# Optimization experiments

Hardware: AMD Instinct MI355X
Metric: run time of the kernel (lower is better)

The kernel has to match this reference:

```python
import jax, jax.numpy as jnp
import numpy as np

EMBED = 768
HEADS = 12
HEAD_DIM = EMBED // HEADS
RANK = 16
EPS = 1e-6
SCALE = 1.0 / np.sqrt(HEAD_DIM)


def setup_inputs() -> dict:
    key = jax.random.key(0)
    ks = jax.random.split(key, 12)
    B, S = 4, 1024
    hidden_states = jax.random.normal(ks[0], (B, S, EMBED), dtype=jnp.float32)
    attention_mask = jnp.zeros((B, 1, 1, S), dtype=jnp.float32)
    w = lambda k: jax.random.normal(k, (EMBED, EMBED), dtype=jnp.float32) * 0.02
    b = lambda k: jax.random.normal(k, (EMBED,), dtype=jnp.float32) * 0.02
    A = jax.random.normal(ks[9], (HEADS, HEAD_DIM, RANK), dtype=jnp.float32) * 0.05
    return {
        "hidden_states": hidden_states,
        "attention_mask": attention_mask,
        "Wq": w(ks[1]), "bq": b(ks[2]),
        "Wk": w(ks[3]), "bk": b(ks[4]),
        "Wv": w(ks[5]), "bv": b(ks[6]),
        "Wo": w(ks[7]), "bo": b(ks[8]),
        "A": A,
    }


def reference(hidden_states, attention_mask, Wq, bq, Wk, bk, Wv, bv, Wo, bo, A):
    B, S, E = hidden_states.shape
    H, D = HEADS, HEAD_DIM

    def proj(W, bias):
        y = hidden_states @ W.T + bias          # (B,S,E), torch Linear: x W^T + b
        return y.reshape(B, S, H, D).transpose(0, 2, 1, 3)  # (B,H,S,D)

    q = proj(Wq, bq)
    k = proj(Wk, bk)
    v = proj(Wv, bv)

    # Low-rank SPD Mahalanobis: G_h = A_h A_h^T + eps*I
    # d^2(x,y) = ||A^T(x-y)||^2 + eps*||x-y||^2 (block-diagonal per batch)
    qA = jnp.einsum("bhsd,hdr->bhsr", q, A)    # (B,H,S,R)
    kA = jnp.einsum("bhsd,hdr->bhsr", k, A)
    qq = jnp.sum(qA * qA, -1) + EPS * jnp.sum(q * q, -1)  # (B,H,S)
    kk = jnp.sum(kA * kA, -1) + EPS * jnp.sum(k * k, -1)
    cross = jnp.einsum("bhsr,bhtr->bhst", qA, kA) + EPS * jnp.einsum("bhsd,bhtd->bhst", q, k)
    d2 = qq[..., :, None] + kk[..., None, :] - 2.0 * cross  # (B,H,S,S)

    scores = -d2 * SCALE + attention_mask      # mask broadcasts (B,1,1,S)
    weights = jax.nn.softmax(scores, axis=-1)  # dropout p is identity in eval
    ctx = jnp.einsum("bhst,bhtd->bhsd", weights, v)
    ctx = ctx.transpose(0, 2, 1, 3).reshape(B, S, E)
    return ctx @ Wo.T + bo
```

## Files before the change

kernel.cpp:

```cpp
#include <hip/hip_runtime.h>

typedef __attribute__((ext_vector_type(8))) short s16x8;
typedef __attribute__((ext_vector_type(4))) float f32x4;
typedef __attribute__((ext_vector_type(4))) unsigned int u32x4;
typedef __attribute__((ext_vector_type(2))) unsigned int u32x2;
typedef unsigned short u16;
typedef unsigned int u32;
typedef unsigned long long u64;

__device__ __forceinline__ u16 f2bf(float f) {
  u32 u = __float_as_uint(f);
  u32 r = u + 0x7fffu + ((u >> 16) & 1u);
  return (u16)(r >> 16);
}
__device__ __forceinline__ float bf2f(u16 h) {
  return __uint_as_float(((u32)h) << 16);
}

typedef __attribute__((address_space(3))) char lds_char_t;
typedef __attribute__((address_space(1))) const char glb_char_t;
__device__ __forceinline__ void gl2lds16(const void* g, void* l) {
  __builtin_amdgcn_global_load_lds((glb_char_t*)g, (lds_char_t*)l, 16, 0, 0);
}

#define HS_N 3145728
#define W_N  589824
#define LOG2E 1.44269504f

__global__ __launch_bounds__(256) void convert_kernel(
    const float* __restrict__ hs, const float* __restrict__ wq, const float* __restrict__ wk,
    const float* __restrict__ wv, const float* __restrict__ wo,
    const float* __restrict__ bq, const float* __restrict__ bk, const float* __restrict__ bv,
    u16* __restrict__ hsb, u16* __restrict__ wqkvb, u16* __restrict__ wob,
    float* __restrict__ biasqkv)
{
  int t = blockIdx.x * 256 + threadIdx.x;
  long i = (long)t * 8;
  const float* src;
  u16* dst;
  if (i < HS_N)              { src = hs + i;                  dst = hsb + i; }
  else if (i < HS_N + W_N)   { src = wq + (i - HS_N);         dst = wqkvb + (i - HS_N); }
  else if (i < HS_N + 2*W_N) { src = wk + (i - HS_N - W_N);   dst = wqkvb + (i - HS_N); }
  else if (i < HS_N + 3*W_N) { src = wv + (i - HS_N - 2*W_N); dst = wqkvb + (i - HS_N); }
  else                       { src = wo + (i - HS_N - 3*W_N); dst = wob + (i - HS_N - 3*W_N); }
  float4 a = ((const float4*)src)[0];
  float4 b = ((const float4*)src)[1];
  uint4 o;
  o.x = (u32)f2bf(a.x) | ((u32)f2bf(a.y) << 16);
  o.y = (u32)f2bf(a.z) | ((u32)f2bf(a.w) << 16);
  o.z = (u32)f2bf(b.x) | ((u32)f2bf(b.y) << 16);
  o.w = (u32)f2bf(b.z) | ((u32)f2bf(b.w) << 16);
  *(uint4*)dst = o;
  if (t < 2304) biasqkv[t] = (t < 768) ? bq[t] : ((t < 1536) ? bk[t - 768] : bv[t - 1536]);
}

template<int MODE>
__global__ __launch_bounds__(256, 2) void gemm_bt(
    const u16* __restrict__ A, const u16* __restrict__ Bt, const float* __restrict__ bias,
    float* __restrict__ outF, u16* __restrict__ Qb, u16* __restrict__ Kb, u16* __restrict__ Vtb)
{
  constexpr int NT = (MODE == 0) ? 18 : 6;
  constexpr int CPX = NT * 64 / 8;

  __shared__ __align__(16) char sm[73728];
  char* const smA = sm;
  char* const smB = sm + 24576;

  const int tid = threadIdx.x;
  const int lane = tid & 63;
  const int w = tid >> 6;
  const int l15 = lane & 15, g = lane >> 4;
  const int wid = (blockIdx.x & 7) * CPX + (blockIdx.x >> 3);
  const int bx = wid % NT, by = wid / NT;
  const int mBase = by * 64;
  const int nBase = bx * 128;
  const int wr = w >> 1, wc = w & 1;
  const int mW = wr * 32, nW = wc * 64;

  f32x4 zero = {0.f, 0.f, 0.f, 0.f};
  f32x4 acc[2][4];
  #pragma unroll
  for (int i = 0; i < 2; i++)
    #pragma unroll
    for (int j = 0; j < 4; j++) acc[i][j] = zero;

  const u16* Arow = A + (long)mBase * 768;
  const u16* Brow = Bt + (long)nBase * 768;

  auto stage = [&](int c, int kb) {
    const int k0 = c * 64;
    #pragma unroll
    for (int i = 0; i < 2; i++) {
      int o = (i * 256 + tid) * 16;
      int r = o >> 7;
      int sl = ((o >> 4) & 7) ^ (r & 7);
      gl2lds16(Arow + (long)r * 768 + k0 + sl * 8,
               smA + kb * 8192 + i * 4096 + w * 1024);
    }
    #pragma unroll
    for (int i = 0; i < 4; i++) {
      int o = (i * 256 + tid) * 16;
      int r = o >> 7;
      int sl = ((o >> 4) & 7) ^ (r & 7);
      gl2lds16(Brow + (long)r * 768 + k0 + sl * 8,
               smB + kb * 16384 + i * 4096 + w * 1024);
    }
  };

  auto compute = [&](int kb) {
    const char* bufA = smA + kb * 8192;
    const char* bufB = smB + kb * 16384;
    #pragma unroll
    for (int kh = 0; kh < 2; kh++) {
      s16x8 af[2], bf[4];
      #pragma unroll
      for (int mi = 0; mi < 2; mi++) {
        int R = mW + mi * 16 + l15;
        af[mi] = *(const s16x8*)(bufA + R * 128 + (((kh * 4 + g) ^ (l15 & 7)) << 4));
      }
      #pragma unroll
      for (int ni = 0; ni < 4; ni++) {
        int R = nW + ni * 16 + l15;
        bf[ni] = *(const s16x8*)(bufB + R * 128 + (((kh * 4 + g) ^ (l15 & 7)) << 4));
      }
      #pragma unroll
      for (int mi = 0; mi < 2; mi++)
        #pragma unroll
        for (int ni = 0; ni < 4; ni++)
          acc[mi][ni] = __builtin_amdgcn_mfma_f32_16x16x32_bf16(af[mi], bf[ni], acc[mi][ni], 0, 0, 0);
    }
  };

  auto body = [&](int c, int kb, int kbn) {
    if (c < 11) { stage(c + 1, kbn); asm volatile("s_waitcnt vmcnt(6)" ::: "memory"); }
    else        { asm volatile("s_waitcnt vmcnt(0)" ::: "memory"); }
    asm volatile("s_barrier" ::: "memory");
    compute(kb);
  };

  stage(0, 0);
  #pragma unroll 1
  for (int cc = 0; cc < 4; cc++) {
    body(cc * 3,     0, 1);
    body(cc * 3 + 1, 1, 2);
    body(cc * 3 + 2, 2, 0);
  }
  __syncthreads();

  const int b_ = mBase >> 10;
  const int s0b = mBase & 1023;

  if constexpr (MODE == 1) {
    #pragma unroll
    for (int mi = 0; mi < 2; mi++)
      #pragma unroll
      for (int ni = 0; ni < 4; ni++) {
        int n = nBase + nW + ni * 16 + l15;
        int m0 = mBase + mW + mi * 16 + g * 4;
        float bb = bias[n];
        outF[(long)m0 * 768 + n]       = acc[mi][ni][0] + bb;
        outF[(long)(m0 + 1) * 768 + n] = acc[mi][ni][1] + bb;
        outF[(long)(m0 + 2) * 768 + n] = acc[mi][ni][2] + bb;
        outF[(long)(m0 + 3) * 768 + n] = acc[mi][ni][3] + bb;
      }
  } else {
    const int typ = bx / 6;
    if (typ < 2) {
      u16* qk = (typ == 0) ? Qb : Kb;
      #pragma unroll
      for (int mi = 0; mi < 2; mi++)
        #pragma unroll
        for (int ni = 0; ni < 4; ni++) {
          int n = nBase + nW + ni * 16 + l15;
          int hn = n - typ * 768;
          int h = hn >> 6, d = hn & 63;
          long bh = (long)b_ * 12 + h;
          int s0 = s0b + mW + mi * 16 + g * 4;
          float bb = bias[n];
          u16* dst = qk + (bh << 16) + ((long)s0 << 6) + d;
          dst[0]   = f2bf(acc[mi][ni][0] + bb);
          dst[64]  = f2bf(acc[mi][ni][1] + bb);
          dst[128] = f2bf(acc[mi][ni][2] + bb);
          dst[192] = f2bf(acc[mi][ni][3] + bb);
        }
    } else {
      u16* ct = (u16*)sm;
      #pragma unroll
      for (int mi = 0; mi < 2; mi++)
        #pragma unroll
        for (int ni = 0; ni < 4; ni++) {
          int nr = nW + ni * 16 + l15;
          int mr = mW + mi * 16 + g * 4;
          float bb = bias[nBase + nr];
          u32 lo = (u32)f2bf(acc[mi][ni][0] + bb) | ((u32)f2bf(acc[mi][ni][1] + bb) << 16);
          u32 hi = (u32)f2bf(acc[mi][ni][2] + bb) | ((u32)f2bf(acc[mi][ni][3] + bb) << 16);
          *(u64*)(ct + nr * 72 + mr) = (u64)lo | ((u64)hi << 32);
        }
      __syncthreads();
      int dr = tid >> 1, part = tid & 1;
      int hn = (bx - 12) * 128 + dr;
      int h = hn >> 6, d = hn & 63;
      long bh = (long)b_ * 12 + h;
      u16* dst = Vtb + (bh << 16) + (d << 10) + s0b + part * 32;
      const u16* srl = ct + dr * 72 + part * 32;
      #pragma unroll
      for (int i = 0; i < 4; i++)
        *(uint4*)(dst + i * 8) = *(const uint4*)(srl + i * 8);
    }
  }
}

__global__ __launch_bounds__(256) void qk_ext_kernel(
    const u16* __restrict__ Qb, const u16* __restrict__ Kb, const float* __restrict__ Am,
    const float* __restrict__ mask, u16* __restrict__ qAe, u16* __restrict__ kAe,
    float* __restrict__ beta2)
{
  __shared__ __align__(16) float AhL[1024];
  const bool isK = blockIdx.x >= 192;
  const int rb = blockIdx.x * 256 - (isK ? 49152 : 0);
  const int h = (rb >> 10) % 12;
  const int row = rb + threadIdx.x;
  const int bh = row >> 10;
  const int s = row & 1023;
  const int b_ = bh / 12;

  ((float4*)AhL)[threadIdx.x] = ((const float4*)(Am + h * 1024))[threadIdx.x];

  const u16* src = (isK ? Kb : Qb) + ((long)row << 6);
  union { uint4 v4[8]; u32 u[32]; } c;
  #pragma unroll
  for (int i = 0; i < 8; i++) c.v4[i] = ((const uint4*)src)[i];

  __syncthreads();

  float acc[16];
  #pragma unroll
  for (int r = 0; r < 16; r++) acc[r] = 0.f;
  float s2 = 0.f;
  #pragma unroll
  for (int d = 0; d < 64; d++) {
    u32 wd = c.u[d >> 1];
    float qd = bf2f((u16)((d & 1) ? (wd >> 16) : (wd & 0xffffu)));
    s2 += qd * qd;
    #pragma unroll
    for (int r4 = 0; r4 < 4; r4++) {
      f32x4 a4 = *(const f32x4*)&AhL[d * 16 + r4 * 4];
      acc[r4 * 4 + 0] += qd * a4[0];
      acc[r4 * 4 + 1] += qd * a4[1];
      acc[r4 * 4 + 2] += qd * a4[2];
      acc[r4 * 4 + 3] += qd * a4[3];
    }
  }

  union { u16 us[128]; uint4 v4[16]; } o;
  const float sA = isK ? 1.0f : 0.25f * LOG2E;
  const float sQ = isK ? 1e-3f : 0.25e-3f * LOG2E;
  #pragma unroll
  for (int r = 0; r < 16; r++) o.us[r] = f2bf(acc[r] * sA);
  #pragma unroll
  for (int d = 0; d < 64; d++) {
    u32 wd = c.u[d >> 1];
    float qd = bf2f((u16)((d & 1) ? (wd >> 16) : (wd & 0xffffu)));
    o.us[16 + d] = f2bf(qd * sQ);
  }
  #pragma unroll
  for (int j = 80; j < 128; j++) o.us[j] = 0;

  u16* dst = (isK ? kAe : qAe) + ((long)row << 7);
  #pragma unroll
  for (int i = 0; i < 16; i++) ((uint4*)dst)[i] = o.v4[i];

  if (isK) {
    float kk = 1e-6f * s2;
    #pragma unroll
    for (int r = 0; r < 16; r++) kk += acc[r] * acc[r];
    beta2[row] = LOG2E * (-0.125f * kk + mask[(b_ << 10) + s]);
  }
}

__global__ __launch_bounds__(128, 2) void attn_kernel(
    const u16* __restrict__ qAe, const u16* __restrict__ kAe, const u16* __restrict__ Vtb,
    const float* __restrict__ beta2, u16* __restrict__ ctxb)
{
  const int tid = threadIdx.x;
  const int lane = tid & 63;
  const int w = tid >> 6;
  const int l15 = lane & 15, g = lane >> 4;
  const int wid = ((int)blockIdx.x & 7) * 96 + ((int)blockIdx.x >> 3);
  const int bh = wid >> 4;
  const int qt = wid & 15;
  const int q0 = qt * 64 + w * 32;

  __shared__ __align__(16) char sm[46080];
  char* const kb0  = sm;
  char* const kb1  = sm + 16384;
  char* const Pw   = sm + 32768 + w * 4608;
  float* const Blds = (float*)(sm + 41984);

  const u16* qbase = qAe + ((long)(bh * 1024 + q0) << 7);
  const u16* kbase = kAe + ((long)bh << 17);
  const u16* vbase = Vtb + ((long)bh << 16);
  const float* betab = beta2 + (bh << 10);

  u32x4 bqv[2][3];
  #pragma unroll
  for (int qf = 0; qf < 2; qf++)
    #pragma unroll
    for (int ks = 0; ks < 3; ks++) {
      const u16* a = qbase + ((qf * 16 + l15) << 7) + ks * 32 + g * 8;
      asm volatile("global_load_dwordx4 %0, %1, off" : "=v"(bqv[qf][ks]) : "v"(a));
    }
  #pragma unroll
  for (int i = 0; i < 4; i++)
    gl2lds16(betab + i * 256 + lane * 4, (char*)Blds + i * 1024);

  auto stageK = [&](int c, char* buf) {
    const int t0 = c * 64;
    #pragma unroll
    for (int i2 = 0; i2 < 8; i2++) {
      int i = w * 8 + i2;
      int r = i * 4 + (lane >> 4);
      int col = ((lane & 15) ^ (r & 7)) * 8;
      gl2lds16(kbase + (long)(t0 + r) * 128 + col, buf + i * 1024);
    }
  };
  auto loadV = [&](int c, u32x4 (&dst)[8]) {
    const int t0 = c * 64;
    #pragma unroll
    for (int ks2 = 0; ks2 < 2; ks2++)
      #pragma unroll
      for (int df = 0; df < 4; df++) {
        const u16* a = vbase + ((df * 16 + l15) << 10) + t0 + ks2 * 32 + g * 8;
        asm volatile("global_load_dwordx4 %0, %1, off" : "=v"(dst[ks2 * 4 + df]) : "v"(a));
      }
  };

  f32x4 zero = {0.f, 0.f, 0.f, 0.f};
  f32x4 cacc[2][4];
  #pragma unroll
  for (int a = 0; a < 2; a++)
    #pragma unroll
    for (int b = 0; b < 4; b++) cacc[a][b] = zero;
  float rsum[2] = {0.f, 0.f};
  u32x4 vb[8];

  stageK(0, kb0);

  std::integral_constant<bool, false> Ff;
  std::integral_constant<bool, true>  Tt;

  auto iter = [&](auto LASTC, int c, const char* bufc, char* bufn) {
    constexpr bool LAST = decltype(LASTC)::value;
    loadV(c, vb);
    asm volatile("s_waitcnt vmcnt(8)" ::: "memory");
    asm volatile("s_barrier" ::: "memory");
    __builtin_amdgcn_sched_barrier(0);
    if constexpr (!LAST) stageK(c + 1, bufn);
    f32x4 sacc[4][2];
    #pragma unroll
    for (int tf = 0; tf < 4; tf++) { sacc[tf][0] = zero; sacc[tf][1] = zero; }
    #pragma unroll
    for (int tf = 0; tf < 4; tf++)
      #pragma unroll
      for (int ks = 0; ks < 3; ks++) {
        s16x8 ak = *(const s16x8*)(bufc + (tf * 16 + l15) * 256 +
                                   ((ks * 64 + g * 16) ^ ((l15 & 7) << 4)));
        s16x8 b0 = __builtin_bit_cast(s16x8, bqv[0][ks]);
        s16x8 b1 = __builtin_bit_cast(s16x8, bqv[1][ks]);
        sacc[tf][0] = __builtin_amdgcn_mfma_f32_16x16x32_bf16(ak, b0, sacc[tf][0], 0, 0, 0);
        sacc[tf][1] = __builtin_amdgcn_mfma_f32_16x16x32_bf16(ak, b1, sacc[tf][1], 0, 0, 0);
      }
    if constexpr (!LAST) asm volatile("s_waitcnt vmcnt(8)" ::: "memory");
    else                 asm volatile("s_waitcnt vmcnt(0)" ::: "memory");
    __builtin_amdgcn_sched_barrier(0);
    #pragma unroll
    for (int tf = 0; tf < 4; tf++) {
      f32x4 bb = *(const f32x4*)((const char*)Blds + c * 256 + tf * 64 + g * 16);
      #pragma unroll
      for (int qf = 0; qf < 2; qf++) {
        float e0, e1, e2, e3;
        asm("v_exp_f32 %0, %1" : "=v"(e0) : "v"(sacc[tf][qf][0] + bb[0]));
        asm("v_exp_f32 %0, %1" : "=v"(e1) : "v"(sacc[tf][qf][1] + bb[1]));
        asm("v_exp_f32 %0, %1" : "=v"(e2) : "v"(sacc[tf][qf][2] + bb[2]));
        asm("v_exp_f32 %0, %1" : "=v"(e3) : "v"(sacc[tf][qf][3] + bb[3]));
        rsum[qf] += (e0 + e1) + (e2 + e3);
        u32 p01, p23;
        asm("v_cvt_pk_bf16_f32 %0, %1, %2" : "=v"(p01) : "v"(e0), "v"(e1));
        asm("v_cvt_pk_bf16_f32 %0, %1, %2" : "=v"(p23) : "v"(e2), "v"(e3));
        u32x2 pk = {p01, p23};
        *(u32x2*)(Pw + (qf * 16 + l15) * 144 + tf * 32 + g * 8) = pk;
      }
    }
    #pragma unroll
    for (int qf = 0; qf < 2; qf++)
      #pragma unroll
      for (int ks2 = 0; ks2 < 2; ks2++) {
        s16x8 ap = *(const s16x8*)(Pw + (qf * 16 + l15) * 144 + ks2 * 64 + g * 16);
        #pragma unroll
        for (int df = 0; df < 4; df++) {
          s16x8 bv = __builtin_bit_cast(s16x8, vb[ks2 * 4 + df]);
          cacc[qf][df] = __builtin_amdgcn_mfma_f32_16x16x32_bf16(ap, bv, cacc[qf][df], 0, 0, 0);
        }
      }
  };

  #pragma unroll 1
  for (int c2 = 0; c2 < 7; c2++) {
    iter(Ff, 2 * c2,     kb0, kb1);
    iter(Ff, 2 * c2 + 1, kb1, kb0);
  }
  iter(Ff, 14, kb0, kb1);
  iter(Tt, 15, kb1, kb0);

  #pragma unroll
  for (int qf = 0; qf < 2; qf++) {
    rsum[qf] += __shfl_xor(rsum[qf], 16);
    rsum[qf] += __shfl_xor(rsum[qf], 32);
  }
  const int b_ = bh / 12, h = bh % 12;
  #pragma unroll
  for (int qf = 0; qf < 2; qf++) {
    #pragma unroll
    for (int j = 0; j < 4; j++) {
      float rs = __shfl(rsum[qf], g * 4 + j);
      float rinv = 1.0f / rs;
      int qg = q0 + qf * 16 + g * 4 + j;
      long base = ((long)(b_ * 1024 + qg)) * 768 + h * 64;
      #pragma unroll
      for (int df = 0; df < 4; df++)
        ctxb[base + df * 16 + l15] = f2bf(cacc[qf][df][j] * rinv);
    }
  }
}

extern "C" void kernel_launch(void* const* d_in, const int* in_sizes, int n_in,
                              void* d_out, int out_size, void* d_ws, size_t ws_size,
                              hipStream_t stream)
{
  (void)in_sizes; (void)n_in; (void)out_size; (void)ws_size;
  const float* hs   = (const float*)d_in[0];
  const float* mask = (const float*)d_in[1];
  const float* Wq   = (const float*)d_in[2];
  const float* bq   = (const float*)d_in[3];
  const float* Wk   = (const float*)d_in[4];
  const float* bk   = (const float*)d_in[5];
  const float* Wv   = (const float*)d_in[6];
  const float* bv   = (const float*)d_in[7];
  const float* Wo   = (const float*)d_in[8];
  const float* bo   = (const float*)d_in[9];
  const float* Am   = (const float*)d_in[10];
  float* out = (float*)d_out;

  char* p = (char*)d_ws;
  u16* hsb      = (u16*)p;   p += 6291456;
  u16* wqkvb    = (u16*)p;   p += 3538944;
  u16* wob      = (u16*)p;   p += 1179648;
  float* biasqkv= (float*)p; p += 9216;
  u16* Qb       = (u16*)p;   p += 6291456;
  u16* Kb       = (u16*)p;   p += 6291456;
  u16* Vtb      = (u16*)p;   p += 6291456;
  u16* qAeb     = (u16*)p;   p += 12582912;
  u16* kAeb     = (u16*)p;   p += 12582912;
  float* beta2  = (float*)p; p += 196608;
  u16* ctxb     = (u16*)p;   p += 6291456;

  convert_kernel<<<2688, 256, 0, stream>>>(hs, Wq, Wk, Wv, Wo, bq, bk, bv,
                                           hsb, wqkvb, wob, biasqkv);
  gemm_bt<0><<<1152, 256, 0, stream>>>(hsb, wqkvb, biasqkv,
                                       nullptr, Qb, Kb, Vtb);
  qk_ext_kernel<<<384, 256, 0, stream>>>(Qb, Kb, Am, mask, qAeb, kAeb, beta2);
  attn_kernel<<<768, 128, 0, stream>>>(qAeb, kAeb, Vtb, beta2, ctxb);
  gemm_bt<1><<<384, 256, 0, stream>>>(ctxb, wob, bo, out,
                                      nullptr, nullptr, nullptr);
}
```

Before: 95.13 us.

## Split attention key range across wave pairs and reduce partials through LDS

Each attention block now runs four waves: two wave pairs each process half of the key sequence for the same 64 queries, using per-pair double-buffered K tiles and smaller 32-key chunks. Partial context accumulators and row sums from the second pair are written to LDS and added by the first pair before normalization and store. This doubles the waves in flight to better hide memory and MFMA latency. In exchange it adds a cross-wave reduction, extra barriers, and smaller per-iteration MFMA work.

```diff
diff --git a/kernel.cpp b/kernel.cpp
--- a/kernel.cpp
+++ b/kernel.cpp
@@ -278,28 +278,29 @@
   }
 }
 
-__global__ __launch_bounds__(128, 2) void attn_kernel(
+__global__ __launch_bounds__(256, 3) void attn_kernel(
     const u16* __restrict__ qAe, const u16* __restrict__ kAe, const u16* __restrict__ Vtb,
     const float* __restrict__ beta2, u16* __restrict__ ctxb)
 {
   const int tid = threadIdx.x;
   const int lane = tid & 63;
   const int w = tid >> 6;
+  const int p = w >> 1, qh = w & 1;
   const int l15 = lane & 15, g = lane >> 4;
   const int wid = ((int)blockIdx.x & 7) * 96 + ((int)blockIdx.x >> 3);
   const int bh = wid >> 4;
   const int qt = wid & 15;
-  const int q0 = qt * 64 + w * 32;
-
-  __shared__ __align__(16) char sm[46080];
-  char* const kb0  = sm;
-  char* const kb1  = sm + 16384;
-  char* const Pw   = sm + 32768 + w * 4608;
-  float* const Blds = (float*)(sm + 41984);
+  const int q0 = qt * 64 + qh * 32;
+
+  __shared__ __align__(16) char sm[47360];
+  char* const Kh    = sm + p * 16384;
+  char* const Pw    = sm + 32768 + w * 2560;
+  float* const Blds = (float*)(sm + 43008);
+  float* const rsLds= (float*)(sm + 47104);
 
   const u16* qbase = qAe + ((long)(bh * 1024 + q0) << 7);
-  const u16* kbase = kAe + ((long)bh << 17);
-  const u16* vbase = Vtb + ((long)bh << 16);
+  const u16* kbase = kAe + ((long)(bh * 1024 + p * 512) << 7);
+  const u16* vbase = Vtb + ((long)bh << 16) + p * 512;
   const float* betab = beta2 + (bh << 10);
 
   u32x4 bqv[2][3];
@@ -310,29 +311,25 @@
       const u16* a = qbase + ((qf * 16 + l15) << 7) + ks * 32 + g * 8;
       asm volatile("global_load_dwordx4 %0, %1, off" : "=v"(bqv[qf][ks]) : "v"(a));
     }
-  #pragma unroll
-  for (int i = 0; i < 4; i++)
-    gl2lds16(betab + i * 256 + lane * 4, (char*)Blds + i * 1024);
+  gl2lds16(betab + w * 256 + lane * 4, (char*)Blds + w * 1024);
 
   auto stageK = [&](int c, char* buf) {
-    const int t0 = c * 64;
-    #pragma unroll
-    for (int i2 = 0; i2 < 8; i2++) {
-      int i = w * 8 + i2;
+    const int t0 = c * 32;
+    #pragma unroll
+    for (int i2 = 0; i2 < 4; i2++) {
+      int i = qh * 4 + i2;
       int r = i * 4 + (lane >> 4);
       int col = ((lane & 15) ^ (r & 7)) * 8;
       gl2lds16(kbase + (long)(t0 + r) * 128 + col, buf + i * 1024);
     }
   };
-  auto loadV = [&](int c, u32x4 (&dst)[8]) {
-    const int t0 = c * 64;
-    #pragma unroll
-    for (int ks2 = 0; ks2 < 2; ks2++)
-      #pragma unroll
-      for (int df = 0; df < 4; df++) {
-        const u16* a = vbase + ((df * 16 + l15) << 10) + t0 + ks2 * 32 + g * 8;
-        asm volatile("global_load_dwordx4 %0, %1, off" : "=v"(dst[ks2 * 4 + df]) : "v"(a));
-      }
+  auto loadV = [&](int c, u32x4 (&dst)[4]) {
+    const int t0 = c * 32;
+    #pragma unroll
+    for (int df = 0; df < 4; df++) {
+      const u16* a = vbase + ((df * 16 + l15) << 10) + t0 + g * 8;
+      asm volatile("global_load_dwordx4 %0, %1, off" : "=v"(dst[df]) : "v"(a));
+    }
   };
 
   f32x4 zero = {0.f, 0.f, 0.f, 0.f};
@@ -342,25 +339,26 @@
     #pragma unroll
     for (int b = 0; b < 4; b++) cacc[a][b] = zero;
   float rsum[2] = {0.f, 0.f};
-  u32x4 vb[8];
-
-  stageK(0, kb0);
+  u32x4 vb[4];
+
+  stageK(0, Kh);
 
   std::integral_constant<bool, false> Ff;
   std::integral_constant<bool, true>  Tt;
 
-  auto iter = [&](auto LASTC, int c, const char* bufc, char* bufn) {
+  auto iter = [&](auto LASTC, int c) {
     constexpr bool LAST = decltype(LASTC)::value;
+    const char* bufc = Kh + (c & 1) * 8192;
+    char* bufn = Kh + ((c + 1) & 1) * 8192;
     loadV(c, vb);
-    asm volatile("s_waitcnt vmcnt(8)" ::: "memory");
+    asm volatile("s_waitcnt vmcnt(4)" ::: "memory");
     asm volatile("s_barrier" ::: "memory");
     __builtin_amdgcn_sched_barrier(0);
     if constexpr (!LAST) stageK(c + 1, bufn);
-    f32x4 sacc[4][2];
-    #pragma unroll
-    for (int tf = 0; tf < 4; tf++) { sacc[tf][0] = zero; sacc[tf][1] = zero; }
-    #pragma unroll
-    for (int tf = 0; tf < 4; tf++)
+    f32x4 sacc[2][2];
+    sacc[0][0] = zero; sacc[0][1] = zero; sacc[1][0] = zero; sacc[1][1] = zero;
+    #pragma unroll
+    for (int tf = 0; tf < 2; tf++)
       #pragma unroll
       for (int ks = 0; ks < 3; ks++) {
         s16x8 ak = *(const s16x8*)(bufc + (tf * 16 + l15) * 256 +
@@ -370,12 +368,12 @@
         sacc[tf][0] = __builtin_amdgcn_mfma_f32_16x16x32_bf16(ak, b0, sacc[tf][0], 0, 0, 0);
         sacc[tf][1] = __builtin_amdgcn_mfma_f32_16x16x32_bf16(ak, b1, sacc[tf][1], 0, 0, 0);
       }
-    if constexpr (!LAST) asm volatile("s_waitcnt vmcnt(8)" ::: "memory");
+    if constexpr (!LAST) asm volatile("s_waitcnt vmcnt(4)" ::: "memory");
     else                 asm volatile("s_waitcnt vmcnt(0)" ::: "memory");
     __builtin_amdgcn_sched_barrier(0);
     #pragma unroll
-    for (int tf = 0; tf < 4; tf++) {
-      f32x4 bb = *(const f32x4*)((const char*)Blds + c * 256 + tf * 64 + g * 16);
+    for (int tf = 0; tf < 2; tf++) {
+      f32x4 bb = *(const f32x4*)((const char*)Blds + (p * 16 + c) * 128 + tf * 64 + g * 16);
       #pragma unroll
       for (int qf = 0; qf < 2; qf++) {
         float e0, e1, e2, e3;
@@ -388,47 +386,67 @@
         asm("v_cvt_pk_bf16_f32 %0, %1, %2" : "=v"(p01) : "v"(e0), "v"(e1));
         asm("v_cvt_pk_bf16_f32 %0, %1, %2" : "=v"(p23) : "v"(e2), "v"(e3));
         u32x2 pk = {p01, p23};
-        *(u32x2*)(Pw + (qf * 16 + l15) * 144 + tf * 32 + g * 8) = pk;
-      }
-    }
-    #pragma unroll
-    for (int qf = 0; qf < 2; qf++)
-      #pragma unroll
-      for (int ks2 = 0; ks2 < 2; ks2++) {
-        s16x8 ap = *(const s16x8*)(Pw + (qf * 16 + l15) * 144 + ks2 * 64 + g * 16);
-        #pragma unroll
-        for (int df = 0; df < 4; df++) {
-          s16x8 bv = __builtin_bit_cast(s16x8, vb[ks2 * 4 + df]);
-          cacc[qf][df] = __builtin_amdgcn_mfma_f32_16x16x32_bf16(ap, bv, cacc[qf][df], 0, 0, 0);
-        }
-      }
+        *(u32x2*)(Pw + (qf * 16 + l15) * 80 + tf * 32 + g * 8) = pk;
+      }
+    }
+    #pragma unroll
+    for (int qf = 0; qf < 2; qf++) {
+      s16x8 ap = *(const s16x8*)(Pw + (qf * 16 + l15) * 80 + g * 16);
+      #pragma unroll
+      for (int df = 0; df < 4; df++) {
+        s16x8 bv = __builtin_bit_cast(s16x8, vb[df]);
+        cacc[qf][df] = __builtin_amdgcn_mfma_f32_16x16x32_bf16(ap, bv, cacc[qf][df], 0, 0, 0);
+      }
+    }
   };
 
   #pragma unroll 1
   for (int c2 = 0; c2 < 7; c2++) {
-    iter(Ff, 2 * c2,     kb0, kb1);
-    iter(Ff, 2 * c2 + 1, kb1, kb0);
-  }
-  iter(Ff, 14, kb0, kb1);
-  iter(Tt, 15, kb1, kb0);
+    iter(Ff, 2 * c2);
+    iter(Ff, 2 * c2 + 1);
+  }
+  iter(Ff, 14);
+  iter(Tt, 15);
 
   #pragma unroll
   for (int qf = 0; qf < 2; qf++) {
     rsum[qf] += __shfl_xor(rsum[qf], 16);
     rsum[qf] += __shfl_xor(rsum[qf], 32);
   }
-  const int b_ = bh / 12, h = bh % 12;
-  #pragma unroll
-  for (int qf = 0; qf < 2; qf++) {
-    #pragma unroll
-    for (int j = 0; j < 4; j++) {
-      float rs = __shfl(rsum[qf], g * 4 + j);
-      float rinv = 1.0f / rs;
-      int qg = q0 + qf * 16 + g * 4 + j;
-      long base = ((long)(b_ * 1024 + qg)) * 768 + h * 64;
+  __syncthreads();
+  float* red = (float*)sm;
+  if (p == 1) {
+    #pragma unroll
+    for (int qf = 0; qf < 2; qf++)
       #pragma unroll
       for (int df = 0; df < 4; df++)
-        ctxb[base + df * 16 + l15] = f2bf(cacc[qf][df][j] * rinv);
+        #pragma unroll
+        for (int j = 0; j < 4; j++)
+          red[(qh * 32 + qf * 16 + g * 4 + j) * 68 + df * 16 + l15] = cacc[qf][df][j];
+    if (g == 0) {
+      rsLds[qh * 32 + l15] = rsum[0];
+      rsLds[qh * 32 + 16 + l15] = rsum[1];
+    }
+  }
+  __syncthreads();
+  if (p == 0) {
+    const int b_ = bh / 12, h = bh % 12;
+    #pragma unroll
+    for (int qf = 0; qf < 2; qf++) {
+      float rt = rsum[qf] + rsLds[qh * 32 + qf * 16 + l15];
+      #pragma unroll
+      for (int j = 0; j < 4; j++) {
+        float rs = __shfl(rt, g * 4 + j);
+        float rinv = 1.0f / rs;
+        int qg = q0 + qf * 16 + g * 4 + j;
+        long base = ((long)(b_ * 1024 + qg)) * 768 + h * 64;
+        #pragma unroll
+        for (int df = 0; df < 4; df++) {
+          float v = cacc[qf][df][j] +
+                    red[(qh * 32 + qf * 16 + g * 4 + j) * 68 + df * 16 + l15];
+          ctxb[base + df * 16 + l15] = f2bf(v * rinv);
+        }
+      }
     }
   }
 }
@@ -469,7 +487,7 @@
   gemm_bt<0><<<1152, 256, 0, stream>>>(hsb, wqkvb, biasqkv,
                                        nullptr, Qb, Kb, Vtb);
   qk_ext_kernel<<<384, 256, 0, stream>>>(Qb, Kb, Am, mask, qAeb, kAeb, beta2);
-  attn_kernel<<<768, 128, 0, stream>>>(qAeb, kAeb, Vtb, beta2, ctxb);
+  attn_kernel<<<768, 256, 0, stream>>>(qAeb, kAeb, Vtb, beta2, ctxb);
   gemm_bt<1><<<384, 256, 0, stream>>>(ctxb, wob, bo, out,
                                       nullptr, nullptr, nullptr);
 }
```

New measurement: 97.63 us. 2.6% more time.
